# Kernel tuning notes

Hardware: AMD Instinct MI355X
Metric: run time of the kernel (lower is better)

The kernel has to match this reference:

```python
import jax, jax.numpy as jnp
import numpy as np

D_IN = 1024
D_OUT = 1024
NUM_HEADS = 16
HEAD_DIM = D_OUT // NUM_HEADS


def setup_inputs() -> dict:
    key = jax.random.key(0)
    ks = jax.random.split(key, 6)
    b, T = 2, 2048
    scale = 0.02
    x = jax.random.normal(ks[0], (b, T, D_IN), dtype=jnp.float32)
    Wq = jax.random.normal(ks[1], (D_IN, D_OUT), dtype=jnp.float32) * scale
    Wk = jax.random.normal(ks[2], (D_IN, D_OUT), dtype=jnp.float32) * scale
    Wv = jax.random.normal(ks[3], (D_IN, D_OUT), dtype=jnp.float32) * scale
    Wo = jax.random.normal(ks[4], (D_OUT, D_OUT), dtype=jnp.float32) * scale
    bo = jnp.zeros((D_OUT,), dtype=jnp.float32)
    return {"x": x, "Wq": Wq, "Wk": Wk, "Wv": Wv, "Wo": Wo, "bo": bo}


def reference(x, Wq, Wk, Wv, Wo, bo):
    b, T, _ = x.shape
    H, Dh = NUM_HEADS, HEAD_DIM
    # projections: [b,T,d_out] -> [b,H,T,Dh]
    q = (x @ Wq).reshape(b, T, H, Dh).transpose(0, 2, 1, 3)
    k = (x @ Wk).reshape(b, T, H, Dh).transpose(0, 2, 1, 3)
    v = (x @ Wv).reshape(b, T, H, Dh).transpose(0, 2, 1, 3)
    # scores: [b,H,T,T]
    att = jnp.einsum('bhqd,bhkd->bhqk', q, k)
    causal = jnp.triu(jnp.ones((T, T), dtype=bool), k=1)
    att = jnp.where(causal, -jnp.inf, att)
    att = jax.nn.softmax(att / np.sqrt(Dh).astype(np.float32), axis=-1)
    # dropout p=0.0 -> identity
    y = jnp.einsum('bhqk,bhkd->bhqd', att, v)
    y = y.transpose(0, 2, 1, 3).reshape(b, T, H * Dh)
    return y @ Wo + bo
```

## Files before the change

kernel.cpp:

```cpp
#include <hip/hip_runtime.h>

#define T_   2048
#define DM   1024
#define H_   16
#define DH   64

typedef unsigned short u16;
typedef unsigned int u32;
typedef __attribute__((ext_vector_type(8))) short bf16x8;
typedef __attribute__((ext_vector_type(8))) unsigned short u16x8;
typedef __attribute__((ext_vector_type(4))) float f32x4;
typedef __attribute__((ext_vector_type(16))) float f32x16;
typedef __attribute__((ext_vector_type(2))) unsigned int u32x2;

static __device__ __forceinline__ u16 f2b(float f) {
  unsigned int u = __builtin_bit_cast(unsigned int, f);
  u += 0x7fff + ((u >> 16) & 1);
  return (u16)(u >> 16);
}

static __device__ __forceinline__ u32 cvtpk(float a, float b) {
  u32 d;
  asm("v_cvt_pk_bf16_f32 %0, %1, %2" : "=v"(d) : "v"(a), "v"(b));
  return d;
}

static __device__ __forceinline__ void gll16(const void* g, void* l) {
  __builtin_amdgcn_global_load_lds(
      (const __attribute__((address_space(1))) unsigned int*)g,
      (__attribute__((address_space(3))) unsigned int*)l, 16, 0, 0);
}

#define RAWBAR()                                   \
  {                                                \
    asm volatile("" ::: "memory");                 \
    __builtin_amdgcn_s_barrier();                  \
    asm volatile("" ::: "memory");                 \
  }

__global__ __launch_bounds__(256) void k_cvt(
    const float* __restrict__ x, u16* __restrict__ xb,
    const float* __restrict__ Wq, const float* __restrict__ Wk,
    const float* __restrict__ Wv, const float* __restrict__ Wo,
    u16* __restrict__ oq, u16* __restrict__ ok, u16* __restrict__ ov,
    u16* __restrict__ oo) {
  __shared__ u16 tile[64][65];
  const int z = blockIdx.z;
  if (z == 4) {
    const int b = blockIdx.y * 16 + blockIdx.x;
#pragma unroll
    for (int it = 0; it < 8; ++it) {
      const int i = b * 16384 + it * 2048 + threadIdx.x * 8;
      float4 a = *(const float4*)(x + i);
      float4 c = *(const float4*)(x + i + 4);
      u16x8 r;
      r[0] = f2b(a.x); r[1] = f2b(a.y); r[2] = f2b(a.z); r[3] = f2b(a.w);
      r[4] = f2b(c.x); r[5] = f2b(c.y); r[6] = f2b(c.z); r[7] = f2b(c.w);
      *(u16x8*)(xb + i) = r;
    }
    return;
  }
  const float* W; u16* Wt;
  if (z == 0)      { W = Wq; Wt = oq; }
  else if (z == 1) { W = Wk; Wt = ok; }
  else if (z == 2) { W = Wv; Wt = ov; }
  else             { W = Wo; Wt = oo; }
  const float wsc = (z == 0) ? 0.1803368801111204f : 1.0f;
  int k0 = blockIdx.x * 64, n0 = blockIdx.y * 64;
  int r = threadIdx.x >> 2, c0 = (threadIdx.x & 3) * 16;
  const float* src = W + (k0 + r) * DM + n0 + c0;
#pragma unroll
  for (int e = 0; e < 16; e += 4) {
    float4 v = *(const float4*)(src + e);
    tile[r][c0 + e + 0] = f2b(v.x * wsc);
    tile[r][c0 + e + 1] = f2b(v.y * wsc);
    tile[r][c0 + e + 2] = f2b(v.z * wsc);
    tile[r][c0 + e + 3] = f2b(v.w * wsc);
  }
  __syncthreads();
  u16x8 a, b;
#pragma unroll
  for (int e = 0; e < 8; ++e) a[e] = tile[c0 + e][r];
#pragma unroll
  for (int e = 0; e < 8; ++e) b[e] = tile[c0 + 8 + e][r];
  u16* dst = Wt + (n0 + r) * DM + k0 + c0;
  *(u16x8*)dst = a;
  *(u16x8*)(dst + 8) = b;
}

__global__ __launch_bounds__(256) void k_qkv(
    const u16* __restrict__ X, const u16* __restrict__ Wqt,
    const u16* __restrict__ Wkt, const u16* __restrict__ Wvt,
    u16* __restrict__ Qg, u16* __restrict__ Kg, u16* __restrict__ Vtg) {
  __shared__ char smem[49152];
  const int tid = threadIdx.x, lane = tid & 63, w = tid >> 6;
  const int frow = lane & 15, fk = lane >> 4;
  const int wr = (w >> 1) * 64, wc = (w & 1) * 64;
  const int m0 = blockIdx.x * 128;
  const int by = blockIdx.y;
  const int z = by >> 3, n0 = (by & 7) * 128;
  const u16* Wt = (z == 0) ? Wqt : (z == 1) ? Wkt : Wvt;
  const u16* Ap = X + m0 * DM;
  const u16* Bp = Wt + n0 * DM;
  const int sro = lane >> 2;
  const int sce = ((lane & 3) ^ ((lane >> 3) & 3)) << 3;

  const u16* pa0 = Ap + (w * 16 + sro) * DM + sce;
  const u16* pa1 = Ap + ((w + 4) * 16 + sro) * DM + sce;
  const u16* pb0 = Bp + (w * 16 + sro) * DM + sce;
  const u16* pb1 = Bp + ((w + 4) * 16 + sro) * DM + sce;
  const int ldsA0 = w * 1024, ldsA1 = (w + 4) * 1024;

  int aoff[4], boff[4];
#pragma unroll
  for (int mi = 0; mi < 4; ++mi) {
    const int rho = wr + mi * 16 + frow;
    aoff[mi] = rho * 64 + ((fk ^ ((rho >> 1) & 3)) << 4);
  }
#pragma unroll
  for (int ni = 0; ni < 4; ++ni) {
    const int rho = wc + ni * 16 + frow;
    boff[ni] = 8192 + rho * 64 + ((fk ^ ((rho >> 1) & 3)) << 4);
  }

  f32x4 acc[4][4];
#pragma unroll
  for (int mi = 0; mi < 4; ++mi)
#pragma unroll
    for (int ni = 0; ni < 4; ++ni) acc[mi][ni] = (f32x4){0.f, 0.f, 0.f, 0.f};

#define STAGEJ(OFS, BUF)                                                     \
  {                                                                          \
    gll16(pa0 + (OFS), (BUF) + ldsA0);                                       \
    gll16(pa1 + (OFS), (BUF) + ldsA1);                                       \
    gll16(pb0 + (OFS), (BUF) + 8192 + ldsA0);                                \
    gll16(pb1 + (OFS), (BUF) + 8192 + ldsA1);                                \
  }

  STAGEJ(0, smem)
  STAGEJ(32, smem + 16384)
  asm volatile("s_waitcnt vmcnt(4)" ::: "memory");
  RAWBAR();

  for (int j = 0; j < 32; ++j) {
    char* cur = smem + (j % 3) * 16384;
    char* nxt = smem + ((j + 2) % 3) * 16384;
    if (j < 30) { STAGEJ((j + 2) * 32, nxt) }
    bf16x8 a[4], b[4];
#pragma unroll
    for (int mi = 0; mi < 4; ++mi)
      a[mi] = *(const bf16x8*)(cur + aoff[mi]);
#pragma unroll
    for (int ni = 0; ni < 4; ++ni)
      b[ni] = *(const bf16x8*)(cur + boff[ni]);
    __builtin_amdgcn_s_setprio(1);
#pragma unroll
    for (int mi = 0; mi < 4; ++mi)
#pragma unroll
      for (int ni = 0; ni < 4; ++ni)
        acc[mi][ni] = __builtin_amdgcn_mfma_f32_16x16x32_bf16(
            a[mi], b[ni], acc[mi][ni], 0, 0, 0);
    __builtin_amdgcn_s_setprio(0);
    if (j < 30) { asm volatile("s_waitcnt vmcnt(4)" ::: "memory"); }
    else        { asm volatile("s_waitcnt vmcnt(0)" ::: "memory"); }
    RAWBAR();
  }
#undef STAGEJ

  if (z < 2) {
    u16* out = (z == 0) ? Qg : Kg;
#pragma unroll
    for (int mi = 0; mi < 4; ++mi)
#pragma unroll
      for (int ni = 0; ni < 4; ++ni)
#pragma unroll
        for (int r = 0; r < 4; ++r) {
          int m = m0 + wr + mi * 16 + fk * 4 + r;
          int nl = n0 + wc + ni * 16 + frow;
          int b = m >> 11, t = m & 2047, h = nl >> 6, d = nl & 63;
          out[((b * H_ + h) * T_ + t) * DH + d] = f2b(acc[mi][ni][r]);
        }
  } else {
    u16* Tl = (u16*)smem;
#pragma unroll
    for (int ni = 0; ni < 4; ++ni) {
      const int n = wc + ni * 16 + frow;
#pragma unroll
      for (int mi = 0; mi < 4; ++mi)
#pragma unroll
        for (int r = 0; r < 4; ++r)
          Tl[n * 136 + wr + mi * 16 + fk * 4 + r] = f2b(acc[mi][ni][r]);
    }
    __syncthreads();
    const int n = tid >> 1, c0 = (tid & 1) * 64;
    const int ng = n0 + n, h = ng >> 6, d = ng & 63;
    const int b = m0 >> 11;
    const int tb = (m0 & 2047) + c0;
    u16* dst = Vtg + ((b * H_ + h) * DH + d) * T_ + tb;
#pragma unroll
    for (int e = 0; e < 8; ++e)
      *(u16x8*)(dst + e * 8) = *(const u16x8*)(Tl + n * 136 + c0 + e * 8);
  }
}

__global__ __launch_bounds__(256) void k_out(
    const u16* __restrict__ Y, const u16* __restrict__ Wot,
    const float* __restrict__ bo, float* __restrict__ out) {
  __shared__ char smem[24576];
  const int tid = threadIdx.x, lane = tid & 63, w = tid >> 6;
  const int frow = lane & 15, fk = lane >> 4;
  const int wr = (w >> 1) * 32, wc = (w & 1) * 64;
  const int m0 = blockIdx.x * 64, n0 = blockIdx.y * 128;
  const u16* Ap = Y + m0 * DM;
  const u16* Bp = Wot + n0 * DM;
  const int sro = lane >> 2;
  const int sce = ((lane & 3) ^ ((lane >> 3) & 3)) << 3;

  f32x4 acc[2][4];
#pragma unroll
  for (int mi = 0; mi < 2; ++mi)
#pragma unroll
    for (int ni = 0; ni < 4; ++ni) acc[mi][ni] = (f32x4){0.f, 0.f, 0.f, 0.f};

#define STAGEO(K0, BUF)                                                      \
  {                                                                          \
    gll16(Ap + (w * 16 + sro) * DM + (K0) + sce, (BUF) + w * 1024);          \
    _Pragma("unroll") for (int c = 0; c < 2; ++c) {                          \
      const int g = w + c * 4;                                               \
      gll16(Bp + (g * 16 + sro) * DM + (K0) + sce, (BUF) + 4096 + g * 1024); \
    }                                                                        \
  }

  STAGEO(0, smem)
  asm volatile("s_waitcnt vmcnt(0)" ::: "memory");
  __syncthreads();

  for (int j = 0; j < 32; ++j) {
    char* cur = smem + (j & 1) * 12288;
    char* nxt = smem + ((j + 1) & 1) * 12288;
    if (j < 31) { STAGEO((j + 1) * 32, nxt) }
    bf16x8 a[2], b[4];
#pragma unroll
    for (int mi = 0; mi < 2; ++mi) {
      const int rho = wr + mi * 16 + frow;
      a[mi] = *(const bf16x8*)(cur + rho * 64 + ((fk ^ ((rho >> 1) & 3)) << 4));
    }
#pragma unroll
    for (int ni = 0; ni < 4; ++ni) {
      const int rho = wc + ni * 16 + frow;
      b[ni] = *(const bf16x8*)(cur + 4096 + rho * 64 +
                               ((fk ^ ((rho >> 1) & 3)) << 4));
    }
    __builtin_amdgcn_s_setprio(1);
#pragma unroll
    for (int mi = 0; mi < 2; ++mi)
#pragma unroll
      for (int ni = 0; ni < 4; ++ni)
        acc[mi][ni] = __builtin_amdgcn_mfma_f32_16x16x32_bf16(
            a[mi], b[ni], acc[mi][ni], 0, 0, 0);
    __builtin_amdgcn_s_setprio(0);
    __syncthreads();
  }
#undef STAGEO

#pragma unroll
  for (int mi = 0; mi < 2; ++mi)
#pragma unroll
    for (int ni = 0; ni < 4; ++ni)
#pragma unroll
      for (int r = 0; r < 4; ++r) {
        int m = m0 + wr + mi * 16 + fk * 4 + r;
        int n = n0 + wc + ni * 16 + frow;
        out[m * DM + n] = acc[mi][ni][r] + bo[n];
      }
}

__global__ __launch_bounds__(256) void k_attn(
    const u16* __restrict__ Qg, const u16* __restrict__ Kg,
    const u16* __restrict__ Vtg, u16* __restrict__ Yg) {
  __shared__ char smem[32768];
  const int bh = blockIdx.x;
  const int qt = 63 - blockIdx.y;
  const int q0 = qt * 32;
  const int tid = threadIdx.x, w = tid >> 6, lane = tid & 63;
  const int hi = lane >> 5, qq = lane & 31;
  const u16* Qb = Qg + bh * (T_ * DH);
  const u16* Kb = Kg + bh * (T_ * DH);
  const u16* Vb = Vtg + bh * (DH * T_);
  const int qrow = q0 + qq;
  char* Kbuf = smem + w * 8192;
  char* Vbuf = Kbuf + 4096;

  bf16x8 qf[4];
#pragma unroll
  for (int kb = 0; kb < 4; ++kb)
    qf[kb] = *(const bf16x8*)(Qb + qrow * DH + kb * 16 + hi * 8);

  f32x16 o0, o1;
#pragma unroll
  for (int r = 0; r < 16; ++r) { o0[r] = 0.f; o1[r] = 0.f; }
  float lp = 0.f;

  const int nt = qt + 1;
  const int kro = lane >> 3;
  const int kce = ((lane & 7) ^ kro) << 3;
  const int vro = lane >> 2;
  const int vce = ((lane & 3) ^ ((vro >> 1) & 3)) << 3;
  const int vs = (qq >> 1) & 3;

  if (w < nt) {
    const int j0w = w * 32;
#pragma unroll
    for (int g = 0; g < 4; ++g)
      gll16(Kb + (j0w + g * 8 + kro) * DH + kce, Kbuf + g * 1024);
#pragma unroll
    for (int g = 0; g < 4; ++g)
      gll16(Vb + (g * 16 + vro) * T_ + j0w + vce, Vbuf + g * 1024);

    for (int t = w; t < nt; t += 4) {
      const bool st = (t + 4 < nt);
      const int jn = (t + 4) * 32;
      asm volatile("s_waitcnt vmcnt(4)" ::: "memory");
      bf16x8 kf[4];
#pragma unroll
      for (int kb = 0; kb < 4; ++kb)
        kf[kb] = *(const bf16x8*)(
            Kbuf + qq * 128 + (((kb * 2 + hi) ^ (qq & 7)) << 4));
      asm volatile("s_waitcnt lgkmcnt(0)" ::: "memory");
      if (st) {
#pragma unroll
        for (int g = 0; g < 4; ++g)
          gll16(Kb + (jn + g * 8 + kro) * DH + kce, Kbuf + g * 1024);
      }
      f32x16 s0;
#pragma unroll
      for (int r = 0; r < 16; ++r) s0[r] = 0.f;
      __builtin_amdgcn_s_setprio(1);
#pragma unroll
      for (int kb = 0; kb < 4; ++kb)
        s0 = __builtin_amdgcn_mfma_f32_32x32x16_bf16(kf[kb], qf[kb], s0, 0, 0, 0);
      __builtin_amdgcn_s_setprio(0);
      if (t == nt - 1) {
#pragma unroll
        for (int r = 0; r < 16; ++r) {
          const int cr = t * 32 + (r & 3) + 8 * (r >> 2) + 4 * hi;
          if (cr > qrow) s0[r] = -1e30f;
        }
      }
#pragma unroll
      for (int r = 0; r < 16; ++r) s0[r] = __builtin_amdgcn_exp2f(s0[r]);
      bf16x8 pb[2];
#define MKCH(DST, S, RB)                                                     \
  {                                                                          \
    u32 a01 = cvtpk(S[RB + 0], S[RB + 1]);                                   \
    u32 a23 = cvtpk(S[RB + 2], S[RB + 3]);                                   \
    u32 a45 = cvtpk(S[RB + 4], S[RB + 5]);                                   \
    u32 a67 = cvtpk(S[RB + 6], S[RB + 7]);                                   \
    asm volatile("v_permlane32_swap_b32 %0, %1" : "+v"(a01), "+v"(a45));     \
    asm volatile("v_permlane32_swap_b32 %0, %1" : "+v"(a23), "+v"(a67));     \
    u32x4_t t4;                                                              \
    t4[0] = a01; t4[1] = a23; t4[2] = a45; t4[3] = a67;                      \
    DST = __builtin_bit_cast(bf16x8, t4);                                    \
  }
      typedef __attribute__((ext_vector_type(4))) unsigned int u32x4_t;
      MKCH(pb[0], s0, 0)
      MKCH(pb[1], s0, 8)
#undef MKCH
      if (st) { asm volatile("s_waitcnt vmcnt(4)" ::: "memory"); }
      else    { asm volatile("s_waitcnt vmcnt(0)" ::: "memory"); }
      bf16x8 vf[4];
      vf[0] = *(const bf16x8*)(Vbuf + qq * 64 + ((hi ^ vs) << 4));
      vf[1] = *(const bf16x8*)(Vbuf + qq * 64 + (((2 + hi) ^ vs) << 4));
      vf[2] = *(const bf16x8*)(Vbuf + (qq + 32) * 64 + ((hi ^ vs) << 4));
      vf[3] = *(const bf16x8*)(Vbuf + (qq + 32) * 64 + (((2 + hi) ^ vs) << 4));
      asm volatile("s_waitcnt lgkmcnt(0)" ::: "memory");
      if (st) {
#pragma unroll
        for (int g = 0; g < 4; ++g)
          gll16(Vb + (g * 16 + vro) * T_ + jn + vce, Vbuf + g * 1024);
      }
      __builtin_amdgcn_s_setprio(1);
      o0 = __builtin_amdgcn_mfma_f32_32x32x16_bf16(vf[0], pb[0], o0, 0, 0, 0);
      o0 = __builtin_amdgcn_mfma_f32_32x32x16_bf16(vf[1], pb[1], o0, 0, 0, 0);
      o1 = __builtin_amdgcn_mfma_f32_32x32x16_bf16(vf[2], pb[0], o1, 0, 0, 0);
      o1 = __builtin_amdgcn_mfma_f32_32x32x16_bf16(vf[3], pb[1], o1, 0, 0, 0);
      __builtin_amdgcn_s_setprio(0);
#pragma unroll
      for (int stp = 8; stp > 0; stp >>= 1)
#pragma unroll
        for (int r = 0; r < stp; ++r) s0[r] += s0[r + stp];
      lp += s0[0];
    }
  }

  asm volatile("s_waitcnt vmcnt(0)" ::: "memory");
  float* po = (float*)Kbuf;
  float* plp = (float*)Vbuf;
#pragma unroll
  for (int r = 0; r < 16; ++r) po[r * 64 + lane] = o0[r];
  plp[lane] = lp;
  __syncthreads();
  if (w == 0) {
#pragma unroll
    for (int sw = 1; sw < 4; ++sw) {
      const float* ps = (const float*)(smem + sw * 8192);
      lp += ((const float*)(smem + sw * 8192 + 4096))[lane];
#pragma unroll
      for (int r = 0; r < 16; ++r) o0[r] += ps[r * 64 + lane];
    }
  }
  __syncthreads();
#pragma unroll
  for (int r = 0; r < 16; ++r) po[r * 64 + lane] = o1[r];
  __syncthreads();
  if (w == 0) {
#pragma unroll
    for (int sw = 1; sw < 4; ++sw) {
      const float* ps = (const float*)(smem + sw * 8192);
#pragma unroll
      for (int r = 0; r < 16; ++r) o1[r] += ps[r * 64 + lane];
    }
    lp += __shfl_xor(lp, 32);
    const float rl = 1.0f / lp;
    const int obase = ((bh >> 4) * T_ + qrow) * DM + (bh & 15) * DH;
#pragma unroll
    for (int g = 0; g < 4; ++g) {
      u32x2 st;
      st[0] = cvtpk(o0[g * 4 + 0] * rl, o0[g * 4 + 1] * rl);
      st[1] = cvtpk(o0[g * 4 + 2] * rl, o0[g * 4 + 3] * rl);
      *(u32x2*)(Yg + obase + g * 8 + hi * 4) = st;
      st[0] = cvtpk(o1[g * 4 + 0] * rl, o1[g * 4 + 1] * rl);
      st[1] = cvtpk(o1[g * 4 + 2] * rl, o1[g * 4 + 3] * rl);
      *(u32x2*)(Yg + obase + 32 + g * 8 + hi * 4) = st;
    }
  }
}


extern "C" void kernel_launch(void* const* d_in, const int* in_sizes, int n_in,
                              void* d_out, int out_size, void* d_ws,
                              size_t ws_size, hipStream_t stream) {
  const float* x  = (const float*)d_in[0];
  const float* Wq = (const float*)d_in[1];
  const float* Wk = (const float*)d_in[2];
  const float* Wv = (const float*)d_in[3];
  const float* Wo = (const float*)d_in[4];
  const float* bo = (const float*)d_in[5];
  float* out = (float*)d_out;
  char* ws = (char*)d_ws;

  u16* xb  = (u16*)(ws);
  u16* wqt = (u16*)(ws + (8ull << 20));
  u16* wkt = (u16*)(ws + (10ull << 20));
  u16* wvt = (u16*)(ws + (12ull << 20));
  u16* wot = (u16*)(ws + (14ull << 20));
  u16* Qg  = (u16*)(ws + (16ull << 20));
  u16* Kg  = (u16*)(ws + (24ull << 20));
  u16* Vtg = (u16*)(ws + (32ull << 20));
  u16* Yg  = (u16*)(ws + (40ull << 20));

  k_cvt<<<dim3(16, 16, 5), 256, 0, stream>>>(x, xb, Wq, Wk, Wv, Wo,
                                             wqt, wkt, wvt, wot);
  k_qkv<<<dim3(32, 24), 256, 0, stream>>>(xb, wqt, wkt, wvt, Qg, Kg, Vtg);
  k_attn<<<dim3(32, 64), 256, 0, stream>>>(Qg, Kg, Vtg, Yg);
  k_out<<<dim3(64, 8), 256, 0, stream>>>(Yg, wot, bo, out);
}
```

Measured before the change: 103.7 us.

## Triple-buffer output projection GEMM with two-stage global prefetch

The output projection kernel moves from double to triple buffering in shared memory, prefetching two K-steps ahead. Partial vmcnt waits plus a raw barrier replace the full drain and __syncthreads, so loads stay in flight across iterations. Global and LDS address offsets are also hoisted out of the loop. This uses more LDS per block, which may reduce occupancy.

```diff
diff --git a/kernel.cpp b/kernel.cpp
--- a/kernel.cpp
+++ b/kernel.cpp
@@ -206,7 +206,7 @@
 __global__ __launch_bounds__(256) void k_out(
     const u16* __restrict__ Y, const u16* __restrict__ Wot,
     const float* __restrict__ bo, float* __restrict__ out) {
-  __shared__ char smem[24576];
+  __shared__ char smem[36864];
   const int tid = threadIdx.x, lane = tid & 63, w = tid >> 6;
   const int frow = lane & 15, fk = lane >> 4;
   const int wr = (w >> 1) * 32, wc = (w & 1) * 64;
@@ -216,41 +216,52 @@
   const int sro = lane >> 2;
   const int sce = ((lane & 3) ^ ((lane >> 3) & 3)) << 3;
 
+  const u16* pa0 = Ap + (w * 16 + sro) * DM + sce;
+  const u16* pb0 = Bp + (w * 16 + sro) * DM + sce;
+  const u16* pb1 = Bp + ((w + 4) * 16 + sro) * DM + sce;
+  const int ldsG0 = w * 1024, ldsG1 = (w + 4) * 1024;
+
+  int aoff[2], boff[4];
+#pragma unroll
+  for (int mi = 0; mi < 2; ++mi) {
+    const int rho = wr + mi * 16 + frow;
+    aoff[mi] = rho * 64 + ((fk ^ ((rho >> 1) & 3)) << 4);
+  }
+#pragma unroll
+  for (int ni = 0; ni < 4; ++ni) {
+    const int rho = wc + ni * 16 + frow;
+    boff[ni] = 4096 + rho * 64 + ((fk ^ ((rho >> 1) & 3)) << 4);
+  }
+
   f32x4 acc[2][4];
 #pragma unroll
   for (int mi = 0; mi < 2; ++mi)
 #pragma unroll
     for (int ni = 0; ni < 4; ++ni) acc[mi][ni] = (f32x4){0.f, 0.f, 0.f, 0.f};
 
-#define STAGEO(K0, BUF)                                                      \
+#define STAGEO(OFS, BUF)                                                     \
   {                                                                          \
-    gll16(Ap + (w * 16 + sro) * DM + (K0) + sce, (BUF) + w * 1024);          \
-    _Pragma("unroll") for (int c = 0; c < 2; ++c) {                          \
-      const int g = w + c * 4;                                               \
-      gll16(Bp + (g * 16 + sro) * DM + (K0) + sce, (BUF) + 4096 + g * 1024); \
-    }                                                                        \
+    gll16(pa0 + (OFS), (BUF) + ldsG0);                                       \
+    gll16(pb0 + (OFS), (BUF) + 4096 + ldsG0);                                \
+    gll16(pb1 + (OFS), (BUF) + 4096 + ldsG1);                                \
   }
 
   STAGEO(0, smem)
-  asm volatile("s_waitcnt vmcnt(0)" ::: "memory");
-  __syncthreads();
+  STAGEO(32, smem + 12288)
+  asm volatile("s_waitcnt vmcnt(3)" ::: "memory");
+  RAWBAR();
 
   for (int j = 0; j < 32; ++j) {
-    char* cur = smem + (j & 1) * 12288;
-    char* nxt = smem + ((j + 1) & 1) * 12288;
-    if (j < 31) { STAGEO((j + 1) * 32, nxt) }
+    char* cur = smem + (j % 3) * 12288;
+    char* nxt = smem + ((j + 2) % 3) * 12288;
+    if (j < 30) { STAGEO((j + 2) * 32, nxt) }
     bf16x8 a[2], b[4];
 #pragma unroll
-    for (int mi = 0; mi < 2; ++mi) {
-      const int rho = wr + mi * 16 + frow;
-      a[mi] = *(const bf16x8*)(cur + rho * 64 + ((fk ^ ((rho >> 1) & 3)) << 4));
-    }
-#pragma unroll
-    for (int ni = 0; ni < 4; ++ni) {
-      const int rho = wc + ni * 16 + frow;
-      b[ni] = *(const bf16x8*)(cur + 4096 + rho * 64 +
-                               ((fk ^ ((rho >> 1) & 3)) << 4));
-    }
+    for (int mi = 0; mi < 2; ++mi)
+      a[mi] = *(const bf16x8*)(cur + aoff[mi]);
+#pragma unroll
+    for (int ni = 0; ni < 4; ++ni)
+      b[ni] = *(const bf16x8*)(cur + boff[ni]);
     __builtin_amdgcn_s_setprio(1);
 #pragma unroll
     for (int mi = 0; mi < 2; ++mi)
@@ -259,7 +270,9 @@
         acc[mi][ni] = __builtin_amdgcn_mfma_f32_16x16x32_bf16(
             a[mi], b[ni], acc[mi][ni], 0, 0, 0);
     __builtin_amdgcn_s_setprio(0);
-    __syncthreads();
+    if (j < 30) { asm volatile("s_waitcnt vmcnt(3)" ::: "memory"); }
+    else        { asm volatile("s_waitcnt vmcnt(0)" ::: "memory"); }
+    RAWBAR();
   }
 #undef STAGEO
 
```

Result: no change. 103.0 us (-0.7%).
